# Optimization experiments

Measured on AMD Instinct MI355X. Metric: run time of the kernel, lower is better.

The kernel has to match this reference:

```python
import jax, jax.numpy as jnp
import numpy as np

N_NODES = 50000
N_EDGES = 800000
N_GRAPHS = 128


def _gcn_conv(x, W, b, src, dst, n_nodes):
    # PyG GCNConv: h = x @ W; add self-loops; symmetric norm; aggregate; + bias
    h = x @ W  # [N, out]
    loop = jnp.arange(n_nodes, dtype=src.dtype)
    src_all = jnp.concatenate([src, loop])  # source (row)
    dst_all = jnp.concatenate([dst, loop])  # target (col)
    ones = jnp.ones(src_all.shape[0], dtype=h.dtype)
    deg = jax.ops.segment_sum(ones, dst_all, num_segments=n_nodes)  # in-degree w/ self loops
    dis = jnp.where(deg > 0, jax.lax.rsqrt(deg), 0.0)
    norm = dis[src_all] * dis[dst_all]  # [E+N]
    msg = norm[:, None] * h[src_all]  # [E+N, out]
    out = jax.ops.segment_sum(msg, dst_all, num_segments=n_nodes)
    return out + b


def setup_inputs() -> dict:
    key = jax.random.key(0)
    ks = jax.random.split(key, 7)
    x = jax.random.normal(ks[0], (N_NODES, 4), dtype=jnp.float32)
    edge_index = jax.random.randint(ks[1], (2, N_EDGES), 0, N_NODES, dtype=jnp.int64)
    batch = jnp.sort(jax.random.randint(ks[2], (N_NODES,), 0, N_GRAPHS, dtype=jnp.int64))
    # Glorot-ish init for the linear weights, zeros for bias (PyG default)
    W1 = jax.random.normal(ks[3], (4, 64), dtype=jnp.float32) * (1.0 / np.sqrt(4))
    b1 = jnp.zeros((64,), dtype=jnp.float32)
    W2 = jax.random.normal(ks[4], (64, 64), dtype=jnp.float32) * (1.0 / np.sqrt(64))
    b2 = jnp.zeros((64,), dtype=jnp.float32)
    return {"x": x, "edge_index": edge_index, "batch": batch, "num_graphs": N_GRAPHS,
            "W1": W1, "b1": b1, "W2": W2, "b2": b2}


def reference(x, edge_index, batch, num_graphs, W1, b1, W2, b2):
    src, dst = edge_index[0], edge_index[1]
    n = x.shape[0]
    h = jax.nn.relu(_gcn_conv(x, W1, b1, src, dst, n))
    h = jax.nn.relu(_gcn_conv(h, W2, b2, src, dst, n))
    # global_mean_pool: segment mean over graph ids
    sums = jax.ops.segment_sum(h, batch, num_segments=num_graphs)  # [G, 64]
    cnts = jax.ops.segment_sum(jnp.ones((n,), dtype=h.dtype), batch, num_segments=num_graphs)
    return sums / jnp.maximum(cnts, 1.0)[:, None]
```

## Files before the change

kernel.cpp:

```cpp
#include <hip/hip_runtime.h>
#include <hip/hip_fp16.h>

#define NG 128
#define CHUNK 4096

__device__ __forceinline__ int wave_iscan(int v, int lane) {
#pragma unroll
  for (int off = 1; off < 64; off <<= 1) {
    int u = __shfl_up(v, off, 64);
    if (lane >= off) v += u;
  }
  return v;
}


__global__ void bsum_kernel(const int* __restrict__ src, int* __restrict__ bsum, int M) {
  __shared__ int wsum[4];
  int tid = threadIdx.x, lane = tid & 63, wid = tid >> 6;
  int i = blockIdx.x * 256 + tid;
  int v = (i < M) ? src[i] : 0;
  int inc = wave_iscan(v, lane);
  if (lane == 63) wsum[wid] = inc;
  __syncthreads();
  if (tid == 0) bsum[blockIdx.x] = wsum[0] + wsum[1] + wsum[2] + wsum[3];
}

__global__ void bscan_kernel(int* __restrict__ bsum, int nb) {
  __shared__ int wsum[16];
  int tid = threadIdx.x, lane = tid & 63, wid = tid >> 6;
  int v = (tid < nb) ? bsum[tid] : 0;
  int inc = wave_iscan(v, lane);
  if (lane == 63) wsum[wid] = inc;
  __syncthreads();
  if (tid == 0) {
    int a = 0;
#pragma unroll
    for (int w = 0; w < 16; ++w) { int t = wsum[w]; wsum[w] = a; a += t; }
  }
  __syncthreads();
  if (tid < nb) bsum[tid] = inc - v + wsum[wid];
}

__global__ void offadd_kernel(int* __restrict__ off, const int* __restrict__ bsum, int M) {
  __shared__ int wsum[4];
  int tid = threadIdx.x, lane = tid & 63, wid = tid >> 6;
  int i = blockIdx.x * 256 + tid;
  int v = (i < M) ? off[i] : 0;
  int inc = wave_iscan(v, lane);
  if (lane == 63) wsum[wid] = inc;
  __syncthreads();
  if (tid == 0) {
    int a = bsum[blockIdx.x];
#pragma unroll
    for (int w = 0; w < 4; ++w) { int t = wsum[w]; wsum[w] = a; a += t; }
  }
  __syncthreads();
  if (i < M) off[i] = inc - v + wsum[wid];
}


__global__ void hist_kernel(const int* __restrict__ ei, int E, int nblkE, int K,
                            int* __restrict__ off) {
  __shared__ int lh[256];
  int tid = threadIdx.x, blk = blockIdx.x;
  lh[tid] = 0;
  __syncthreads();
  int e0 = blk * CHUNK;
  for (int i = tid; i < CHUNK; i += 256) {
    int e = e0 + i;
    if (e < E) atomicAdd(&lh[ei[E + e] >> 8], 1);
  }
  __syncthreads();
  if (tid < K) off[tid * nblkE + blk] = lh[tid];
}

__global__ void part_kernel(const int* __restrict__ ei, int E, int nblkE, int K,
                            const int* __restrict__ off, int* __restrict__ psrc,
                            unsigned short* __restrict__ pld) {
  __shared__ int lcur[256];
  int tid = threadIdx.x, blk = blockIdx.x;
  if (tid < K) lcur[tid] = off[tid * nblkE + blk];
  __syncthreads();
  int e0 = blk * CHUNK;
  for (int i = tid; i < CHUNK; i += 256) {
    int e = e0 + i;
    if (e < E) {
      int s = ei[e], d = ei[E + e];
      int pos = atomicAdd(&lcur[d >> 8], 1);
      psrc[pos] = s;
      pld[pos] = (unsigned short)(d & 255);
    }
  }
}

__global__ void csr2_kernel(const int* __restrict__ off, int nblkE, int K,
                            const int* __restrict__ psrc,
                            const unsigned short* __restrict__ pld,
                            const float* __restrict__ x, int* __restrict__ deg,
                            int* __restrict__ rowptr, float* __restrict__ dis,
                            float* __restrict__ xs, int* __restrict__ esrc,
                            int N, int E) {
  __shared__ int lcnt[256];
  __shared__ int lcur[256];
  __shared__ int wsum[4];
  int tid = threadIdx.x, b = blockIdx.x;
  int lane = tid & 63, wid = tid >> 6;
  lcnt[tid] = 0;
  __syncthreads();
  int be0 = off[b * nblkE];
  int be1 = (b + 1 < K) ? off[(b + 1) * nblkE] : E;
  for (int i = be0 + tid; i < be1; i += 256) atomicAdd(&lcnt[pld[i]], 1);
  __syncthreads();
  int v = lcnt[tid];
  int inc = wave_iscan(v, lane);
  if (lane == 63) wsum[wid] = inc;
  __syncthreads();
  if (tid == 0) {
    int a = be0;
#pragma unroll
    for (int w = 0; w < 4; ++w) { int t = wsum[w]; wsum[w] = a; a += t; }
  }
  __syncthreads();
  int exc = inc - v + wsum[wid];
  lcur[tid] = exc;
  int node = (b << 8) + tid;
  if (node < N) {
    rowptr[node] = exc;
    deg[node] = v;
    float di = rsqrtf((float)v + 1.0f);
    dis[node] = di;
    float4 xv = ((const float4*)x)[node];
    ((float4*)xs)[node] = make_float4(di * xv.x, di * xv.y, di * xv.z, di * xv.w);
  }
  __syncthreads();
  for (int i = be0 + tid; i < be1; i += 256) {
    int pos = atomicAdd(&lcur[pld[i]], 1);
    esrc[pos] = psrc[i];
  }
}

__global__ void l1_kernel(const int* __restrict__ rowptr, const int* __restrict__ deg,
                          const int* __restrict__ esrc, const float* __restrict__ xs,
                          const float* __restrict__ x, const float* __restrict__ dis,
                          const float* __restrict__ W1, const float* __restrict__ b1,
                          __half* __restrict__ h1p, int N) {
  int tid = threadIdx.x;
  int lane = tid & 63, wid = tid >> 6;
  int d = __builtin_amdgcn_readfirstlane(blockIdx.x * 4 + wid);
  if (d >= N) return;
  float di = dis[d];
  int p = __builtin_amdgcn_readfirstlane(rowptr[d]);
  int n = __builtin_amdgcn_readfirstlane(deg[d]);
  float a0 = 0.f, a1 = 0.f, a2 = 0.f, a3 = 0.f;
  for (int k = lane; k < n; k += 64) {
    int e = esrc[p + k];
    float4 v = ((const float4*)xs)[e];
    a0 += v.x; a1 += v.y; a2 += v.z; a3 += v.w;
  }
  if (lane == 0) {
    float4 xv = ((const float4*)x)[d];
    a0 = fmaf(di, xv.x, a0); a1 = fmaf(di, xv.y, a1);
    a2 = fmaf(di, xv.z, a2); a3 = fmaf(di, xv.w, a3);
  }
#pragma unroll
  for (int off = 1; off < 64; off <<= 1) {
    a0 += __shfl_xor(a0, off, 64);
    a1 += __shfl_xor(a1, off, 64);
    a2 += __shfl_xor(a2, off, 64);
    a3 += __shfl_xor(a3, off, 64);
  }
  a0 *= di; a1 *= di; a2 *= di; a3 *= di;
  float o = b1[lane] + a0 * W1[lane] + a1 * W1[64 + lane] + a2 * W1[128 + lane] + a3 * W1[192 + lane];
  h1p[(long)d * 64 + lane] = __float2half(di * fmaxf(o, 0.0f));
}

__global__ void __launch_bounds__(256)
l2_kernel(const int* __restrict__ rowptr, const int* __restrict__ deg,
          const int* __restrict__ esrc, const __half* __restrict__ h1p,
          const float* __restrict__ dis, const float* __restrict__ W2,
          const float* __restrict__ b2, const int* __restrict__ batch,
          float* __restrict__ gsum, int N) {
  __shared__ float vbuf[4][64];
  __shared__ float obuf[4][64];
  __shared__ int gbuf[4];
  int tid = threadIdx.x;
  int lane = tid & 63, wid = tid >> 6;
  int d0 = blockIdx.x * 4 + wid;
  bool valid = d0 < N;
  int d = __builtin_amdgcn_readfirstlane(valid ? d0 : N - 1);
  float di = dis[d];
  float acc0 = __half2float(h1p[(long)d * 64 + lane]);
  float acc1 = 0.f, acc2 = 0.f, acc3 = 0.f;
  float acc4 = 0.f, acc5 = 0.f, acc6 = 0.f, acc7 = 0.f;
  int p = __builtin_amdgcn_readfirstlane(rowptr[d]);
  int n = __builtin_amdgcn_readfirstlane(deg[d]);
  for (int k = 0; k < n; k += 16) {
    int es[16];
#pragma unroll
    for (int i = 0; i < 16; ++i) {
      int idx = k + i;
      es[i] = esrc[p + ((idx < n) ? idx : (n - 1))];
    }
#pragma unroll
    for (int i = 0; i < 16; ++i) {
      float m = (k + i < n) ? 1.0f : 0.0f;
      float v = __half2float(h1p[(long)es[i] * 64 + lane]);
      switch (i & 7) {
        case 0: acc0 = fmaf(m, v, acc0); break;
        case 1: acc1 = fmaf(m, v, acc1); break;
        case 2: acc2 = fmaf(m, v, acc2); break;
        case 3: acc3 = fmaf(m, v, acc3); break;
        case 4: acc4 = fmaf(m, v, acc4); break;
        case 5: acc5 = fmaf(m, v, acc5); break;
        case 6: acc6 = fmaf(m, v, acc6); break;
        case 7: acc7 = fmaf(m, v, acc7); break;
      }
    }
  }
  float v = di * (((acc0 + acc1) + (acc2 + acc3)) + ((acc4 + acc5) + (acc6 + acc7)));
  vbuf[wid][lane] = v;
  float o = b2[lane];
  const float4* vb4 = (const float4*)vbuf[wid];
#pragma unroll
  for (int kk = 0; kk < 16; ++kk) {
    float4 vv = vb4[kk];
    o = fmaf(vv.x, W2[(kk * 4 + 0) * 64 + lane], o);
    o = fmaf(vv.y, W2[(kk * 4 + 1) * 64 + lane], o);
    o = fmaf(vv.z, W2[(kk * 4 + 2) * 64 + lane], o);
    o = fmaf(vv.w, W2[(kk * 4 + 3) * 64 + lane], o);
  }
  obuf[wid][lane] = fmaxf(o, 0.0f);
  if (lane == 0) gbuf[wid] = valid ? batch[d] : -1;
  __syncthreads();
  if (wid == 0) {
    float s = 0.0f;
    int cur = gbuf[0];
#pragma unroll
    for (int r = 0; r < 4; ++r) {
      int g = gbuf[r];
      if (g != cur) {
        if (cur >= 0) atomicAdd(&gsum[cur * 64 + lane], s);
        s = 0.0f;
        cur = g;
      }
      if (g >= 0) s += obuf[r][lane];
    }
    if (cur >= 0) atomicAdd(&gsum[cur * 64 + lane], s);
  }
}


__device__ __forceinline__ int lbound(const int* __restrict__ a, int n, int v) {
  int lo = 0, hi = n;
  while (lo < hi) {
    int mid = (lo + hi) >> 1;
    if (a[mid] < v) lo = mid + 1; else hi = mid;
  }
  return lo;
}

__global__ void out_kernel(const float* __restrict__ gsum, const int* __restrict__ batch,
                           int N, float* __restrict__ out) {
  int t = blockIdx.x * blockDim.x + threadIdx.x;
  if (t >= NG * 64) return;
  int g = t >> 6;
  int cnt = lbound(batch, N, g + 1) - lbound(batch, N, g);
  out[t] = gsum[t] / fmaxf((float)cnt, 1.0f);
}


extern "C" void kernel_launch(void* const* d_in, const int* in_sizes, int n_in,
                              void* d_out, int out_size, void* d_ws, size_t ws_size,
                              hipStream_t stream) {
  const float* x = (const float*)d_in[0];
  const int* ei = (const int*)d_in[1];
  const int* batch = (const int*)d_in[2];
  const float* W1 = (const float*)d_in[4];
  const float* b1 = (const float*)d_in[5];
  const float* W2 = (const float*)d_in[6];
  const float* b2 = (const float*)d_in[7];

  const int N = in_sizes[0] / 4;
  const int E = in_sizes[1] / 2;
  const int K = (N + 255) >> 8;
  const int nblkE = (E + CHUNK - 1) / CHUNK;
  const int M2 = K * nblkE;
  const int NB2 = (M2 + 255) / 256;

  float* gsum = (float*)d_ws;
  int* deg = (int*)(gsum + 64 * NG);
  int* rowptr = deg + N;
  float* xs = (float*)(rowptr + N);
  float* dis = xs + (long)4 * N;
  __half* h1p = (__half*)(dis + N);
  int* off = (int*)(dis + N + (long)32 * N);
  int* bsum2 = off + M2;
  int* psrc = bsum2 + 1024;
  unsigned short* pld = (unsigned short*)(psrc + E);
  int* esrc = (int*)(pld + E);

  hipMemsetAsync(d_ws, 0, (size_t)64 * NG * 4, stream);

  const int B = 256;
  hist_kernel<<<nblkE, 256, 0, stream>>>(ei, E, nblkE, K, off);
  bsum_kernel<<<NB2, 256, 0, stream>>>(off, bsum2, M2);
  bscan_kernel<<<1, 1024, 0, stream>>>(bsum2, NB2);
  offadd_kernel<<<NB2, 256, 0, stream>>>(off, bsum2, M2);
  part_kernel<<<nblkE, 256, 0, stream>>>(ei, E, nblkE, K, off, psrc, pld);
  csr2_kernel<<<K, 256, 0, stream>>>(off, nblkE, K, psrc, pld, x, deg, rowptr, dis, xs, esrc, N, E);
  l1_kernel<<<(N + 3) / 4, 256, 0, stream>>>(rowptr, deg, esrc, xs, x, dis, W1, b1, h1p, N);
  l2_kernel<<<(N + 3) / 4, 256, 0, stream>>>(rowptr, deg, esrc, h1p, dis, W2, b2, batch, gsum, N);
  out_kernel<<<(NG * 64 + B - 1) / B, B, 0, stream>>>(gsum, batch, N, (float*)d_out);
}
```

Measured before the change: 120.1 us.

## Pack edges, use 16-bit sources, and slice layer-2 gather by feature chunks

Packs source and low destination bits into a single word during partitioning and stores CSR sources as 16-bit indices, which cuts edge traffic. The layer-1 output is stored in eight column slices so that layer-2 aggregation runs as eight passes, each gathering from a small cache-friendly table. The dense W2 transform and pooling move to a separate kernel that reads an fp16 intermediate buffer. The trade-off is 8x more index reads and an extra launch and buffer round trip, and 16-bit indices limit the node count to 65536.

```diff
diff --git a/kernel.cpp b/kernel.cpp
--- a/kernel.cpp
+++ b/kernel.cpp
@@ -75,8 +75,7 @@
 }
 
 __global__ void part_kernel(const int* __restrict__ ei, int E, int nblkE, int K,
-                            const int* __restrict__ off, int* __restrict__ psrc,
-                            unsigned short* __restrict__ pld) {
+                            const int* __restrict__ off, unsigned int* __restrict__ epack) {
   __shared__ int lcur[256];
   int tid = threadIdx.x, blk = blockIdx.x;
   if (tid < K) lcur[tid] = off[tid * nblkE + blk];
@@ -85,20 +84,18 @@
   for (int i = tid; i < CHUNK; i += 256) {
     int e = e0 + i;
     if (e < E) {
-      int s = ei[e], d = ei[E + e];
+      unsigned int s = (unsigned int)ei[e], d = (unsigned int)ei[E + e];
       int pos = atomicAdd(&lcur[d >> 8], 1);
-      psrc[pos] = s;
-      pld[pos] = (unsigned short)(d & 255);
+      epack[pos] = (s << 8) | (d & 255u);
     }
   }
 }
 
 __global__ void csr2_kernel(const int* __restrict__ off, int nblkE, int K,
-                            const int* __restrict__ psrc,
-                            const unsigned short* __restrict__ pld,
+                            const unsigned int* __restrict__ epack,
                             const float* __restrict__ x, int* __restrict__ deg,
                             int* __restrict__ rowptr, float* __restrict__ dis,
-                            float* __restrict__ xs, int* __restrict__ esrc,
+                            float* __restrict__ xs, unsigned short* __restrict__ esrc,
                             int N, int E) {
   __shared__ int lcnt[256];
   __shared__ int lcur[256];
@@ -109,7 +106,7 @@
   __syncthreads();
   int be0 = off[b * nblkE];
   int be1 = (b + 1 < K) ? off[(b + 1) * nblkE] : E;
-  for (int i = be0 + tid; i < be1; i += 256) atomicAdd(&lcnt[pld[i]], 1);
+  for (int i = be0 + tid; i < be1; i += 256) atomicAdd(&lcnt[epack[i] & 255u], 1);
   __syncthreads();
   int v = lcnt[tid];
   int inc = wave_iscan(v, lane);
@@ -134,16 +131,17 @@
   }
   __syncthreads();
   for (int i = be0 + tid; i < be1; i += 256) {
-    int pos = atomicAdd(&lcur[pld[i]], 1);
-    esrc[pos] = psrc[i];
+    unsigned int pk = epack[i];
+    int pos = atomicAdd(&lcur[pk & 255u], 1);
+    esrc[pos] = (unsigned short)(pk >> 8);
   }
 }
 
 __global__ void l1_kernel(const int* __restrict__ rowptr, const int* __restrict__ deg,
-                          const int* __restrict__ esrc, const float* __restrict__ xs,
+                          const unsigned short* __restrict__ esrc, const float* __restrict__ xs,
                           const float* __restrict__ x, const float* __restrict__ dis,
                           const float* __restrict__ W1, const float* __restrict__ b1,
-                          __half* __restrict__ h1p, int N) {
+                          __half* __restrict__ h1ps, int N) {
   int tid = threadIdx.x;
   int lane = tid & 63, wid = tid >> 6;
   int d = __builtin_amdgcn_readfirstlane(blockIdx.x * 4 + wid);
@@ -171,16 +169,57 @@
   }
   a0 *= di; a1 *= di; a2 *= di; a3 *= di;
   float o = b1[lane] + a0 * W1[lane] + a1 * W1[64 + lane] + a2 * W1[128 + lane] + a3 * W1[192 + lane];
-  h1p[(long)d * 64 + lane] = __float2half(di * fmaxf(o, 0.0f));
+  h1ps[(size_t)(lane >> 3) * N * 8 + (size_t)d * 8 + (lane & 7)] =
+      __float2half(di * fmaxf(o, 0.0f));
 }
 
 __global__ void __launch_bounds__(256)
-l2_kernel(const int* __restrict__ rowptr, const int* __restrict__ deg,
-          const int* __restrict__ esrc, const __half* __restrict__ h1p,
-          const float* __restrict__ dis, const float* __restrict__ W2,
-          const float* __restrict__ b2, const int* __restrict__ batch,
-          float* __restrict__ gsum, int N) {
-  __shared__ float vbuf[4][64];
+l2a_kernel(const int* __restrict__ rowptr, const int* __restrict__ deg,
+           const unsigned short* __restrict__ esrc, const __half* __restrict__ h1ps,
+           const float* __restrict__ dis, __half* __restrict__ vbuf, int N) {
+  int tid = threadIdx.x;
+  int lane = tid & 63, wid = tid >> 6;
+  int q = blockIdx.x & 7;
+  int d0 = (blockIdx.x >> 3) * 4 + wid;
+  if (d0 >= N) return;
+  int d = __builtin_amdgcn_readfirstlane(d0);
+  float di = dis[d];
+  const __half* tab = h1ps + (size_t)q * N * 8;
+  int p = __builtin_amdgcn_readfirstlane(rowptr[d]);
+  int n = __builtin_amdgcn_readfirstlane(deg[d]);
+  int fp = lane & 3;
+  float ax = 0.f, ay = 0.f;
+  for (int k = 0; k < n; k += 16) {
+    int idx = k + (lane & 15);
+    int e_l = esrc[p + ((idx < n) ? idx : (n - 1))];
+    int e = __shfl(e_l, lane >> 2, 64);
+    float m = ((k + (lane >> 2)) < n) ? 1.0f : 0.0f;
+    __half2 hv = *(const __half2*)(tab + (size_t)e * 8 + fp * 2);
+    float2 f = __half22float2(hv);
+    ax = fmaf(m, f.x, ax);
+    ay = fmaf(m, f.y, ay);
+  }
+#pragma unroll
+  for (int off = 4; off < 64; off <<= 1) {
+    ax += __shfl_xor(ax, off, 64);
+    ay += __shfl_xor(ay, off, 64);
+  }
+  float2 sf = __half22float2(*(const __half2*)(tab + (size_t)d * 8 + fp * 2));
+  ax = di * (ax + sf.x);
+  ay = di * (ay + sf.y);
+  if (lane < 4) {
+    __half2 r;
+    r.x = __float2half(ax);
+    r.y = __float2half(ay);
+    ((__half2*)vbuf)[(size_t)d * 32 + q * 4 + fp] = r;
+  }
+}
+
+__global__ void __launch_bounds__(256)
+l2b_kernel(const __half* __restrict__ vbuf, const float* __restrict__ W2,
+           const float* __restrict__ b2, const int* __restrict__ batch,
+           float* __restrict__ gsum, int N) {
+  __shared__ float vb[4][64];
   __shared__ float obuf[4][64];
   __shared__ int gbuf[4];
   int tid = threadIdx.x;
@@ -188,39 +227,10 @@
   int d0 = blockIdx.x * 4 + wid;
   bool valid = d0 < N;
   int d = __builtin_amdgcn_readfirstlane(valid ? d0 : N - 1);
-  float di = dis[d];
-  float acc0 = __half2float(h1p[(long)d * 64 + lane]);
-  float acc1 = 0.f, acc2 = 0.f, acc3 = 0.f;
-  float acc4 = 0.f, acc5 = 0.f, acc6 = 0.f, acc7 = 0.f;
-  int p = __builtin_amdgcn_readfirstlane(rowptr[d]);
-  int n = __builtin_amdgcn_readfirstlane(deg[d]);
-  for (int k = 0; k < n; k += 16) {
-    int es[16];
-#pragma unroll
-    for (int i = 0; i < 16; ++i) {
-      int idx = k + i;
-      es[i] = esrc[p + ((idx < n) ? idx : (n - 1))];
-    }
-#pragma unroll
-    for (int i = 0; i < 16; ++i) {
-      float m = (k + i < n) ? 1.0f : 0.0f;
-      float v = __half2float(h1p[(long)es[i] * 64 + lane]);
-      switch (i & 7) {
-        case 0: acc0 = fmaf(m, v, acc0); break;
-        case 1: acc1 = fmaf(m, v, acc1); break;
-        case 2: acc2 = fmaf(m, v, acc2); break;
-        case 3: acc3 = fmaf(m, v, acc3); break;
-        case 4: acc4 = fmaf(m, v, acc4); break;
-        case 5: acc5 = fmaf(m, v, acc5); break;
-        case 6: acc6 = fmaf(m, v, acc6); break;
-        case 7: acc7 = fmaf(m, v, acc7); break;
-      }
-    }
-  }
-  float v = di * (((acc0 + acc1) + (acc2 + acc3)) + ((acc4 + acc5) + (acc6 + acc7)));
-  vbuf[wid][lane] = v;
+  float v = __half2float(vbuf[(size_t)d * 64 + lane]);
+  vb[wid][lane] = v;
   float o = b2[lane];
-  const float4* vb4 = (const float4*)vbuf[wid];
+  const float4* vb4 = (const float4*)vb[wid];
 #pragma unroll
   for (int kk = 0; kk < 16; ++kk) {
     float4 vv = vb4[kk];
@@ -291,13 +301,13 @@
   int* deg = (int*)(gsum + 64 * NG);
   int* rowptr = deg + N;
   float* xs = (float*)(rowptr + N);
-  float* dis = xs + (long)4 * N;
-  __half* h1p = (__half*)(dis + N);
-  int* off = (int*)(dis + N + (long)32 * N);
+  float* dis = xs + (size_t)4 * N;
+  __half* h1ps = (__half*)(dis + N);
+  unsigned short* esrc = (unsigned short*)(dis + N + (size_t)32 * N);
+  int* off = (int*)(esrc + E);
   int* bsum2 = off + M2;
-  int* psrc = bsum2 + 1024;
-  unsigned short* pld = (unsigned short*)(psrc + E);
-  int* esrc = (int*)(pld + E);
+  unsigned int* epack = (unsigned int*)(bsum2 + 1024);
+  __half* vbuf = (__half*)epack;
 
   hipMemsetAsync(d_ws, 0, (size_t)64 * NG * 4, stream);
 
@@ -306,9 +316,10 @@
   bsum_kernel<<<NB2, 256, 0, stream>>>(off, bsum2, M2);
   bscan_kernel<<<1, 1024, 0, stream>>>(bsum2, NB2);
   offadd_kernel<<<NB2, 256, 0, stream>>>(off, bsum2, M2);
-  part_kernel<<<nblkE, 256, 0, stream>>>(ei, E, nblkE, K, off, psrc, pld);
-  csr2_kernel<<<K, 256, 0, stream>>>(off, nblkE, K, psrc, pld, x, deg, rowptr, dis, xs, esrc, N, E);
-  l1_kernel<<<(N + 3) / 4, 256, 0, stream>>>(rowptr, deg, esrc, xs, x, dis, W1, b1, h1p, N);
-  l2_kernel<<<(N + 3) / 4, 256, 0, stream>>>(rowptr, deg, esrc, h1p, dis, W2, b2, batch, gsum, N);
+  part_kernel<<<nblkE, 256, 0, stream>>>(ei, E, nblkE, K, off, epack);
+  csr2_kernel<<<K, 256, 0, stream>>>(off, nblkE, K, epack, x, deg, rowptr, dis, xs, esrc, N, E);
+  l1_kernel<<<(N + 3) / 4, 256, 0, stream>>>(rowptr, deg, esrc, xs, x, dis, W1, b1, h1ps, N);
+  l2a_kernel<<<((N + 3) / 4) * 8, 256, 0, stream>>>(rowptr, deg, esrc, h1ps, dis, vbuf, N);
+  l2b_kernel<<<(N + 3) / 4, 256, 0, stream>>>(vbuf, W2, b2, batch, gsum, N);
   out_kernel<<<(NG * 64 + B - 1) / B, B, 0, stream>>>(gsum, batch, N, (float*)d_out);
 }
```

New measurement: 182.1 us. 1.52x slower.

## Pack partitioned edges into one word and store CSR sources as 16-bit

Applied to the files above, without the earlier changes.

The partition pass now writes a single packed 32-bit word per edge (source shifted left 8, low byte of destination) instead of separate int and ushort arrays. The final CSR source array becomes unsigned short, halving index traffic in csr2, l1 and l2. The l2 gather loop is also unrolled from 16 to 32 edges per batch to get more loads in flight. The 16-bit source indices only work for graphs with at most 65536 nodes, and the larger unroll raises register pressure.

```diff
diff --git a/kernel.cpp b/kernel.cpp
--- a/kernel.cpp
+++ b/kernel.cpp
@@ -75,8 +75,7 @@
 }
 
 __global__ void part_kernel(const int* __restrict__ ei, int E, int nblkE, int K,
-                            const int* __restrict__ off, int* __restrict__ psrc,
-                            unsigned short* __restrict__ pld) {
+                            const int* __restrict__ off, unsigned int* __restrict__ epack) {
   __shared__ int lcur[256];
   int tid = threadIdx.x, blk = blockIdx.x;
   if (tid < K) lcur[tid] = off[tid * nblkE + blk];
@@ -85,20 +84,18 @@
   for (int i = tid; i < CHUNK; i += 256) {
     int e = e0 + i;
     if (e < E) {
-      int s = ei[e], d = ei[E + e];
+      unsigned int s = (unsigned int)ei[e], d = (unsigned int)ei[E + e];
       int pos = atomicAdd(&lcur[d >> 8], 1);
-      psrc[pos] = s;
-      pld[pos] = (unsigned short)(d & 255);
+      epack[pos] = (s << 8) | (d & 255u);
     }
   }
 }
 
 __global__ void csr2_kernel(const int* __restrict__ off, int nblkE, int K,
-                            const int* __restrict__ psrc,
-                            const unsigned short* __restrict__ pld,
+                            const unsigned int* __restrict__ epack,
                             const float* __restrict__ x, int* __restrict__ deg,
                             int* __restrict__ rowptr, float* __restrict__ dis,
-                            float* __restrict__ xs, int* __restrict__ esrc,
+                            float* __restrict__ xs, unsigned short* __restrict__ esrc,
                             int N, int E) {
   __shared__ int lcnt[256];
   __shared__ int lcur[256];
@@ -109,7 +106,7 @@
   __syncthreads();
   int be0 = off[b * nblkE];
   int be1 = (b + 1 < K) ? off[(b + 1) * nblkE] : E;
-  for (int i = be0 + tid; i < be1; i += 256) atomicAdd(&lcnt[pld[i]], 1);
+  for (int i = be0 + tid; i < be1; i += 256) atomicAdd(&lcnt[epack[i] & 255u], 1);
   __syncthreads();
   int v = lcnt[tid];
   int inc = wave_iscan(v, lane);
@@ -134,13 +131,14 @@
   }
   __syncthreads();
   for (int i = be0 + tid; i < be1; i += 256) {
-    int pos = atomicAdd(&lcur[pld[i]], 1);
-    esrc[pos] = psrc[i];
+    unsigned int pk = epack[i];
+    int pos = atomicAdd(&lcur[pk & 255u], 1);
+    esrc[pos] = (unsigned short)(pk >> 8);
   }
 }
 
 __global__ void l1_kernel(const int* __restrict__ rowptr, const int* __restrict__ deg,
-                          const int* __restrict__ esrc, const float* __restrict__ xs,
+                          const unsigned short* __restrict__ esrc, const float* __restrict__ xs,
                           const float* __restrict__ x, const float* __restrict__ dis,
                           const float* __restrict__ W1, const float* __restrict__ b1,
                           __half* __restrict__ h1p, int N) {
@@ -171,12 +169,12 @@
   }
   a0 *= di; a1 *= di; a2 *= di; a3 *= di;
   float o = b1[lane] + a0 * W1[lane] + a1 * W1[64 + lane] + a2 * W1[128 + lane] + a3 * W1[192 + lane];
-  h1p[(long)d * 64 + lane] = __float2half(di * fmaxf(o, 0.0f));
+  h1p[(size_t)d * 64 + lane] = __float2half(di * fmaxf(o, 0.0f));
 }
 
 __global__ void __launch_bounds__(256)
 l2_kernel(const int* __restrict__ rowptr, const int* __restrict__ deg,
-          const int* __restrict__ esrc, const __half* __restrict__ h1p,
+          const unsigned short* __restrict__ esrc, const __half* __restrict__ h1p,
           const float* __restrict__ dis, const float* __restrict__ W2,
           const float* __restrict__ b2, const int* __restrict__ batch,
           float* __restrict__ gsum, int N) {
@@ -189,22 +187,22 @@
   bool valid = d0 < N;
   int d = __builtin_amdgcn_readfirstlane(valid ? d0 : N - 1);
   float di = dis[d];
-  float acc0 = __half2float(h1p[(long)d * 64 + lane]);
+  float acc0 = __half2float(h1p[(size_t)d * 64 + lane]);
   float acc1 = 0.f, acc2 = 0.f, acc3 = 0.f;
   float acc4 = 0.f, acc5 = 0.f, acc6 = 0.f, acc7 = 0.f;
   int p = __builtin_amdgcn_readfirstlane(rowptr[d]);
   int n = __builtin_amdgcn_readfirstlane(deg[d]);
-  for (int k = 0; k < n; k += 16) {
-    int es[16];
-#pragma unroll
-    for (int i = 0; i < 16; ++i) {
+  for (int k = 0; k < n; k += 32) {
+    int es[32];
+#pragma unroll
+    for (int i = 0; i < 32; ++i) {
       int idx = k + i;
       es[i] = esrc[p + ((idx < n) ? idx : (n - 1))];
     }
 #pragma unroll
-    for (int i = 0; i < 16; ++i) {
+    for (int i = 0; i < 32; ++i) {
       float m = (k + i < n) ? 1.0f : 0.0f;
-      float v = __half2float(h1p[(long)es[i] * 64 + lane]);
+      float v = __half2float(h1p[(size_t)es[i] * 64 + lane]);
       switch (i & 7) {
         case 0: acc0 = fmaf(m, v, acc0); break;
         case 1: acc1 = fmaf(m, v, acc1); break;
@@ -291,13 +289,12 @@
   int* deg = (int*)(gsum + 64 * NG);
   int* rowptr = deg + N;
   float* xs = (float*)(rowptr + N);
-  float* dis = xs + (long)4 * N;
+  float* dis = xs + (size_t)4 * N;
   __half* h1p = (__half*)(dis + N);
-  int* off = (int*)(dis + N + (long)32 * N);
+  unsigned short* esrc = (unsigned short*)(dis + N + (size_t)32 * N);
+  int* off = (int*)(esrc + E);
   int* bsum2 = off + M2;
-  int* psrc = bsum2 + 1024;
-  unsigned short* pld = (unsigned short*)(psrc + E);
-  int* esrc = (int*)(pld + E);
+  unsigned int* epack = (unsigned int*)(bsum2 + 1024);
 
   hipMemsetAsync(d_ws, 0, (size_t)64 * NG * 4, stream);
 
@@ -306,8 +303,8 @@
   bsum_kernel<<<NB2, 256, 0, stream>>>(off, bsum2, M2);
   bscan_kernel<<<1, 1024, 0, stream>>>(bsum2, NB2);
   offadd_kernel<<<NB2, 256, 0, stream>>>(off, bsum2, M2);
-  part_kernel<<<nblkE, 256, 0, stream>>>(ei, E, nblkE, K, off, psrc, pld);
-  csr2_kernel<<<K, 256, 0, stream>>>(off, nblkE, K, psrc, pld, x, deg, rowptr, dis, xs, esrc, N, E);
+  part_kernel<<<nblkE, 256, 0, stream>>>(ei, E, nblkE, K, off, epack);
+  csr2_kernel<<<K, 256, 0, stream>>>(off, nblkE, K, epack, x, deg, rowptr, dis, xs, esrc, N, E);
   l1_kernel<<<(N + 3) / 4, 256, 0, stream>>>(rowptr, deg, esrc, xs, x, dis, W1, b1, h1p, N);
   l2_kernel<<<(N + 3) / 4, 256, 0, stream>>>(rowptr, deg, esrc, h1p, dis, W2, b2, batch, gsum, N);
   out_kernel<<<(NG * 64 + B - 1) / B, B, 0, stream>>>(gsum, batch, N, (float*)d_out);
```

Measured after the change: 124.9 us. 4.0% more time.
